# Performance work log

Measured on AMD Instinct MI355X. Metric: run time of the kernel, lower is better.

The kernel has to match this reference:

```python
import jax, jax.numpy as jnp
import numpy as np

N_NODES = 50000
N_EDGES = 800000
N_GRAPHS = 512
D_IN = 128
D_HID = 128
D_OUT = 128
N_CLS = 2


def _deg_inv_sqrt(idx, n):
    deg = jax.ops.segment_sum(jnp.ones(idx.shape[0], jnp.float32), idx, num_segments=n)
    return jnp.where(deg > 0, jax.lax.rsqrt(jnp.maximum(deg, 1.0)), 0.0)


def gcn_conv(x, src, dst, W, b, out_norm, in_norm):
    # DGL GraphConv, norm='both': D_out^{-1/2} on src, sum-aggregate, D_in^{-1/2} on dst, then XW + b
    h = x * out_norm[:, None]                                   # [N, d]
    agg = jax.ops.segment_sum(h[src], dst, num_segments=x.shape[0])  # SpMM: gather + scatter-add
    agg = agg * in_norm[:, None]
    return agg @ W + b


def setup_inputs() -> dict:
    key = jax.random.key(0)
    ks = jax.random.split(key, 8)
    features = jax.random.normal(ks[0], (N_NODES, D_IN), jnp.float32)
    src = jax.random.randint(ks[1], (N_EDGES,), 0, N_NODES, jnp.int32)
    dst = jax.random.randint(ks[2], (N_EDGES,), 0, N_NODES, jnp.int32)
    graph_ids = jnp.sort(jax.random.randint(ks[3], (N_NODES,), 0, N_GRAPHS, jnp.int32))
    W1 = jax.random.normal(ks[4], (D_IN, D_HID), jnp.float32) / np.sqrt(D_IN)
    W2 = jax.random.normal(ks[5], (D_HID, D_OUT), jnp.float32) / np.sqrt(D_HID)
    Wc = jax.random.normal(ks[6], (D_OUT, N_CLS), jnp.float32) / np.sqrt(D_OUT)
    return {
        'features': features, 'src': src, 'dst': dst, 'graph_ids': graph_ids,
        'W1': W1, 'b1': jnp.zeros((D_HID,), jnp.float32),
        'W2': W2, 'b2': jnp.zeros((D_OUT,), jnp.float32),
        'Wc': Wc, 'bc': jnp.zeros((N_CLS,), jnp.float32),
    }


def reference(features, src, dst, graph_ids, W1, b1, W2, b2, Wc, bc):
    n = features.shape[0]
    out_norm = _deg_inv_sqrt(src, n)   # out-degree norm (applied on src side)
    in_norm = _deg_inv_sqrt(dst, n)    # in-degree norm (applied on dst side)
    h = jax.nn.relu(gcn_conv(features, src, dst, W1, b1, out_norm, in_norm))
    h = gcn_conv(h, src, dst, W2, b2, out_norm, in_norm)
    # mean_nodes: segment mean over nodes of each graph
    sums = jax.ops.segment_sum(h, graph_ids, num_segments=N_GRAPHS)          # [G, d]
    cnts = jax.ops.segment_sum(jnp.ones((n,), jnp.float32), graph_ids, num_segments=N_GRAPHS)
    hg = sums / jnp.maximum(cnts, 1.0)[:, None]
    return hg @ Wc + bc
```

## Files before the change

kernel.cpp:

```cpp
#include <hip/hip_runtime.h>
#include <hip/hip_fp16.h>

#define NN 50000
#define NE 800000
#define NG 512
#define DD 128
#define NSB 64
#define SUBN 782
#define SBCAP 14336
#define NB1 512
#define NI4 (NE / 4)
#define CH4 ((NI4 + NB1 - 1) / NB1)
#define F2HB 6250

typedef __attribute__((ext_vector_type(8))) _Float16 f16x8;
typedef __attribute__((ext_vector_type(4))) float f32x4;
typedef int v4i __attribute__((ext_vector_type(4)));

__global__ void k_zero(int* __restrict__ p) {
  p[threadIdx.x] = 0;
}

__global__ __launch_bounds__(256) void k_prep(
    const float* __restrict__ W1, const float* __restrict__ W2,
    const float* __restrict__ Wc, const float* __restrict__ b2,
    const float* __restrict__ bc,
    _Float16* __restrict__ w1hi, _Float16* __restrict__ w1lo,
    float* __restrict__ w2c, float* __restrict__ zc,
    const int* __restrict__ src, const int* __restrict__ dst,
    int* __restrict__ cur_d, int* __restrict__ cur_s,
    unsigned long long* __restrict__ byDst, unsigned short* __restrict__ bySrc,
    const float4* __restrict__ x, uint2* __restrict__ xh) {
  __shared__ int cntd[4][NSB], cnts[4][NSB], based[NSB], bases[NSB];
  __shared__ int wbd[4][NSB], wbs[4][NSB];
  int b = blockIdx.x;
  int tid = threadIdx.x;
  if (b >= 521) {
    int i = (b - 521) * 256 + tid;
    float4 v = x[i];
    __half2 a = __floats2half2_rn(v.x, v.y);
    __half2 c = __floats2half2_rn(v.z, v.w);
    uint2 o;
    o.x = *(unsigned int*)&a;
    o.y = *(unsigned int*)&c;
    xh[i] = o;
  } else if (b < 8) {
    int t = b * 256 + tid;
    int lane = t & 63;
    int grp = t >> 6;
    int kk = grp & 3;
    int nt = grp >> 2;
    int kbase = kk * 32 + ((lane >> 4) << 3);
    int c = nt * 16 + (lane & 15);
#pragma unroll
    for (int j = 0; j < 8; ++j) {
      float v = W1[(kbase + j) * DD + c];
      _Float16 h = (_Float16)v;
      w1hi[t * 8 + j] = h;
      w1lo[t * 8 + j] = (_Float16)(v - (float)h);
    }
  } else if (b == 8) {
    int row = tid >> 1, cc = tid & 1;
    float s = 0.f;
#pragma unroll 8
    for (int c = 0; c < DD; ++c) s += W2[row * DD + c] * Wc[c * 2 + cc];
    w2c[row * 2 + cc] = s;
    if (tid < 2) {
      float bb = 0.f;
      for (int c = 0; c < DD; ++c) bb += b2[c] * Wc[c * 2 + tid];
      zc[tid] = bb + bc[tid];
    }
  } else {
    int w = tid >> 6;
    int i0 = (b - 9) * CH4;
    int i1 = i0 + CH4; if (i1 > NI4) i1 = NI4;
    if (tid < NSB) {
#pragma unroll
      for (int ww = 0; ww < 4; ++ww) { cntd[ww][tid] = 0; cnts[ww][tid] = 0; }
    }
    __syncthreads();
    const v4i* s4 = (const v4i*)src;
    const v4i* d4 = (const v4i*)dst;
    for (int i = i0 + tid; i < i1; i += 256) {
      v4i sv = __builtin_nontemporal_load(&s4[i]);
      v4i dv = __builtin_nontemporal_load(&d4[i]);
#pragma unroll
      for (int k = 0; k < 4; ++k) {
        atomicAdd(&cntd[w][dv[k] / SUBN], 1);
        atomicAdd(&cnts[w][sv[k] / SUBN], 1);
      }
    }
    __syncthreads();
    if (tid < NSB) {
      int run = 0;
#pragma unroll
      for (int ww = 0; ww < 4; ++ww) { wbd[ww][tid] = run; run += cntd[ww][tid]; }
      based[tid] = atomicAdd(&cur_d[tid], run);
#pragma unroll
      for (int ww = 0; ww < 4; ++ww) cntd[ww][tid] = 0;
    } else if (tid < 2 * NSB) {
      int q = tid - NSB;
      int run = 0;
#pragma unroll
      for (int ww = 0; ww < 4; ++ww) { wbs[ww][q] = run; run += cnts[ww][q]; }
      bases[q] = atomicAdd(&cur_s[q], run);
#pragma unroll
      for (int ww = 0; ww < 4; ++ww) cnts[ww][q] = 0;
    }
    __syncthreads();
    for (int i = i0 + tid; i < i1; i += 256) {
      v4i sv = __builtin_nontemporal_load(&s4[i]);
      v4i dv = __builtin_nontemporal_load(&d4[i]);
#pragma unroll
      for (int k = 0; k < 4; ++k) {
        int d = dv[k], s = sv[k];
        int bd = d / SUBN;
        int pd = based[bd] + wbd[w][bd] + atomicAdd(&cntd[w][bd], 1);
        if (pd < SBCAP) byDst[(size_t)bd * SBCAP + pd] = ((unsigned long long)(unsigned)d << 32) | (unsigned)s;
        int bs = s / SUBN;
        int ps = bases[bs] + wbs[w][bs] + atomicAdd(&cnts[w][bs], 1);
        if (ps < SBCAP) bySrc[(size_t)bs * SBCAP + ps] = (unsigned short)(s - bs * SUBN);
      }
    }
  }
}

__global__ __launch_bounds__(1024) void k_csr2(
    const unsigned long long* __restrict__ byDst, const int* __restrict__ cur_d,
    const unsigned short* __restrict__ bySrc, const int* __restrict__ cur_s,
    int* __restrict__ csr, int* __restrict__ row_start, int* __restrict__ deg_in,
    float* __restrict__ in_norm, float* __restrict__ out_norm) {
  __shared__ int hist[SUBN];
  __shared__ int wsum[16];
  int b = blockIdx.x;
  int tid = threadIdx.x;
  if (b < 64) {
    int q = b;
    int nlo = q * SUBN;
    int nhi = nlo + SUBN; if (nhi > NN) nhi = NN;
    int nloc = nhi - nlo;
    for (int i = tid; i < SUBN; i += 1024) hist[i] = 0;
    __syncthreads();
    int m = cur_d[q];
    if (m > SBCAP) m = SBCAP;
    const unsigned long long* bine = byDst + (size_t)q * SBCAP;
    for (int i = tid; i < m; i += 1024) {
      int l = (int)(bine[i] >> 32) - nlo;
      if (l >= 0 && l < nloc) atomicAdd(&hist[l], 1);
    }
    __syncthreads();
    int v = (tid < SUBN) ? hist[tid] : 0;
    int incl = v;
    int lane = tid & 63;
#pragma unroll
    for (int off = 1; off < 64; off <<= 1) {
      int t2 = __shfl_up(incl, off);
      if (lane >= off) incl += t2;
    }
    int wid = tid >> 6;
    if (lane == 63) wsum[wid] = incl;
    __syncthreads();
    if (tid == 0) {
      int run = 0;
      for (int i = 0; i < 16; ++i) { int t = wsum[i]; wsum[i] = run; run += t; }
    }
    __syncthreads();
    int excl = incl - v + wsum[wid];
    if (tid < nloc) {
      deg_in[nlo + tid] = v;
      row_start[nlo + tid] = q * SBCAP + excl;
      in_norm[nlo + tid] = v > 0 ? rsqrtf((float)v) : 0.f;
    }
    __syncthreads();
    if (tid < SUBN) hist[tid] = excl;
    __syncthreads();
    for (int i = tid; i < m; i += 1024) {
      unsigned long long p = bine[i];
      int l = (int)(p >> 32) - nlo;
      if (l >= 0 && l < nloc) {
        int pos = atomicAdd(&hist[l], 1);
        if (pos < SBCAP) csr[(size_t)q * SBCAP + pos] = (int)(unsigned)p;
      }
    }
  } else {
    int q = b - 64;
    int nlo = q * SUBN;
    int nhi = nlo + SUBN; if (nhi > NN) nhi = NN;
    int nloc = nhi - nlo;
    for (int i = tid; i < SUBN; i += 1024) hist[i] = 0;
    __syncthreads();
    int m = cur_s[q];
    if (m > SBCAP) m = SBCAP;
    const unsigned short* bine = bySrc + (size_t)q * SBCAP;
    for (int i = tid; i < m; i += 1024) {
      atomicAdd(&hist[bine[i]], 1);
    }
    __syncthreads();
    for (int i = tid; i < nloc; i += 1024) {
      int od = hist[i];
      out_norm[nlo + i] = od > 0 ? rsqrtf((float)od) : 0.f;
    }
  }
}

__global__ __launch_bounds__(256) void k_agg(
    const __half* __restrict__ x, const int* __restrict__ csr,
    const int* __restrict__ row_start, const int* __restrict__ deg_in,
    const float* __restrict__ out_norm, uint2* __restrict__ agg) {
  int node = blockIdx.x * 4 + (threadIdx.x >> 6);
  int lane = threadIdx.x & 63;
  if (node >= NN) return;
  int n = deg_in[node];
  const int* bk = csr + row_start[node];
  const uint2* xv = (const uint2*)x;
  int half_ = lane >> 5;
  int l32 = lane & 31;
  float4 acc[8];
#pragma unroll
  for (int u = 0; u < 8; ++u) acc[u] = make_float4(0.f, 0.f, 0.f, 0.f);
  for (int c0 = 0; c0 < n; c0 += 64) {
    int nn = n - c0; if (nn > 64) nn = 64;
    int sl = 0; float wl = 0.f;
    if (lane < nn) { sl = bk[c0 + lane]; wl = out_norm[sl]; }
    for (int j = 0; j < nn; j += 16) {
#pragma unroll
      for (int u = 0; u < 8; ++u) {
        int e = j + 2 * u + half_;
        int s = __shfl(sl, e);
        float w = __shfl(wl, e);
        if (e < nn) {
          uint2 raw = xv[(size_t)s * 32 + l32];
          float2 f0 = __half22float2(*(__half2*)&raw.x);
          float2 f1 = __half22float2(*(__half2*)&raw.y);
          acc[u].x += f0.x * w; acc[u].y += f0.y * w;
          acc[u].z += f1.x * w; acc[u].w += f1.y * w;
        }
      }
    }
  }
  float4 a = acc[0];
#pragma unroll
  for (int u = 1; u < 8; ++u) {
    a.x += acc[u].x; a.y += acc[u].y; a.z += acc[u].z; a.w += acc[u].w;
  }
  a.x += __shfl_xor(a.x, 32);
  a.y += __shfl_xor(a.y, 32);
  a.z += __shfl_xor(a.z, 32);
  a.w += __shfl_xor(a.w, 32);
  if (lane < 32) {
    __half2 h0 = __floats2half2_rn(a.x, a.y);
    __half2 h1 = __floats2half2_rn(a.z, a.w);
    uint2 o;
    o.x = *(unsigned int*)&h0;
    o.y = *(unsigned int*)&h1;
    agg[(size_t)node * 32 + l32] = o;
  }
}

__global__ __launch_bounds__(256, 4) void k_gemm1(
    const __half* __restrict__ A, const float* __restrict__ in_norm,
    const float* __restrict__ out_norm,
    const _Float16* __restrict__ Whi, const _Float16* __restrict__ Wlo,
    const float* __restrict__ bias, const float* __restrict__ W2c,
    float2* __restrict__ p) {
  int tid = threadIdx.x;
  int wid = tid >> 6, lane = tid & 63;
  int row0 = blockIdx.x * 64 + wid * 16;
  int ar = row0 + (lane & 15);
  bool rv = ar < NN;
  f16x8 a_[4];
#pragma unroll
  for (int kk = 0; kk < 4; ++kk) {
    if (rv) {
      a_[kk] = *(const f16x8*)((const _Float16*)A + (size_t)ar * DD + kk * 32 + ((lane >> 4) << 3));
    } else {
      a_[kk] = (f16x8){0, 0, 0, 0, 0, 0, 0, 0};
    }
  }
  f32x4 acc[8];
#pragma unroll
  for (int nt = 0; nt < 8; ++nt) acc[nt] = (f32x4){0.f, 0.f, 0.f, 0.f};
#pragma unroll
  for (int nt = 0; nt < 8; ++nt) {
#pragma unroll
    for (int kk = 0; kk < 4; ++kk) {
      f16x8 bh = *(const f16x8*)&Whi[(((nt * 4 + kk) * 64) + lane) * 8];
      f16x8 bl = *(const f16x8*)&Wlo[(((nt * 4 + kk) * 64) + lane) * 8];
      acc[nt] = __builtin_amdgcn_mfma_f32_16x16x32_f16(a_[kk], bh, acc[nt], 0, 0, 0);
      acc[nt] = __builtin_amdgcn_mfma_f32_16x16x32_f16(a_[kk], bl, acc[nt], 0, 0, 0);
    }
  }
  int r4 = (lane >> 4) * 4;
  int c0 = lane & 15;
  float wc0[8], wc1[8], bv[8];
#pragma unroll
  for (int nt = 0; nt < 8; ++nt) {
    int col = nt * 16 + c0;
    wc0[nt] = W2c[col * 2 + 0];
    wc1[nt] = W2c[col * 2 + 1];
    bv[nt] = bias[col];
  }
#pragma unroll
  for (int reg = 0; reg < 4; ++reg) {
    int row = row0 + r4 + reg;
    float inm = (row < NN) ? in_norm[row] : 0.f;
    float v0 = 0.f, v1 = 0.f;
#pragma unroll
    for (int nt = 0; nt < 8; ++nt) {
      float y = acc[nt][reg] * inm + bv[nt];
      y = fmaxf(y, 0.f);
      v0 += y * wc0[nt];
      v1 += y * wc1[nt];
    }
#pragma unroll
    for (int off = 1; off < 16; off <<= 1) {
      v0 += __shfl_xor(v0, off);
      v1 += __shfl_xor(v1, off);
    }
    if (row < NN && c0 == 0) {
      float onm = out_norm[row];
      p[row] = make_float2(v0 * onm, v1 * onm);
    }
  }
}

__global__ __launch_bounds__(256) void k_agg2(
    const float2* __restrict__ p, const int* __restrict__ csr,
    const int* __restrict__ row_start, const int* __restrict__ deg_in,
    const float* __restrict__ in_norm, float2* __restrict__ z) {
  int i = blockIdx.x * 256 + threadIdx.x;
  if (i >= NN) return;
  int n = deg_in[i];
  const int* bk = csr + row_start[i];
  float2 s0 = {0.f, 0.f}, s1 = {0.f, 0.f}, s2 = {0.f, 0.f}, s3 = {0.f, 0.f};
  int j = 0;
  for (; j + 4 <= n; j += 4) {
    int i0 = bk[j], i1 = bk[j + 1], i2 = bk[j + 2], i3 = bk[j + 3];
    float2 q0 = p[i0], q1 = p[i1], q2 = p[i2], q3 = p[i3];
    s0.x += q0.x; s0.y += q0.y;
    s1.x += q1.x; s1.y += q1.y;
    s2.x += q2.x; s2.y += q2.y;
    s3.x += q3.x; s3.y += q3.y;
  }
  for (; j < n; ++j) {
    float2 q = p[bk[j]];
    s0.x += q.x; s0.y += q.y;
  }
  s0.x += s1.x + s2.x + s3.x;
  s0.y += s1.y + s2.y + s3.y;
  float inm = in_norm[i];
  z[i] = make_float2(s0.x * inm, s0.y * inm);
}

__global__ __launch_bounds__(256) void k_pool2(
    const float* __restrict__ z, const int* __restrict__ gid,
    const float* __restrict__ zc, float* __restrict__ out) {
  int g = blockIdx.x * 4 + (threadIdx.x >> 6);
  int lane = threadIdx.x & 63;
  if (g >= NG) return;
  int lo, hi;
  { int a = 0, b = NN; while (a < b) { int m = (a + b) >> 1; if (gid[m] < g) a = m + 1; else b = m; } lo = a; }
  { int a = lo, b = NN; while (a < b) { int m = (a + b) >> 1; if (gid[m] <= g) a = m + 1; else b = m; } hi = a; }
  float s = 0.f;
  int col = lane & 1;
  for (int i = lo + (lane >> 1); i < hi; i += 32) s += z[i * 2 + col];
#pragma unroll
  for (int off = 32; off >= 2; off >>= 1) s += __shfl_down(s, off);
  if (lane < 2) {
    int n = hi - lo;
    out[g * 2 + lane] = s / (float)(n > 0 ? n : 1) + zc[lane];
  }
}

extern "C" void kernel_launch(void* const* d_in, const int* in_sizes, int n_in,
                              void* d_out, int out_size, void* d_ws, size_t ws_size,
                              hipStream_t stream) {
  const float* features = (const float*)d_in[0];
  const int* src = (const int*)d_in[1];
  const int* dst = (const int*)d_in[2];
  const int* gid = (const int*)d_in[3];
  const float* W1 = (const float*)d_in[4];
  const float* b1 = (const float*)d_in[5];
  const float* W2 = (const float*)d_in[6];
  const float* b2 = (const float*)d_in[7];
  const float* Wc = (const float*)d_in[8];
  const float* bc = (const float*)d_in[9];
  float* out = (float*)d_out;

  char* ws = (char*)d_ws;
  size_t off = 0;
  auto take = [&](size_t bytes) {
    char* p = ws + off;
    off = (off + bytes + 255) & ~(size_t)255;
    return p;
  };
  int* cur_d      = (int*)take(NSB * 4);
  int* cur_s      = (int*)take(NSB * 4);
  int* deg_in     = (int*)take((size_t)NN * 4);
  float* out_nrm  = (float*)take((size_t)NN * 4);
  float* in_nrm   = (float*)take((size_t)NN * 4);
  int* row_start  = (int*)take((size_t)NN * 4);
  float* pbuf     = (float*)take((size_t)NN * 2 * 4);
  float* zbuf     = (float*)take((size_t)NN * 2 * 4);
  float* w2c      = (float*)take((size_t)DD * 2 * 4);
  float* zc       = (float*)take(2 * 4);
  unsigned long long* byDst = (unsigned long long*)take((size_t)NSB * SBCAP * 8);
  unsigned short* bySrc = (unsigned short*)take((size_t)NSB * SBCAP * 2);
  int* csr        = (int*)take((size_t)NSB * SBCAP * 4);
  __half* xh      = (__half*)take((size_t)NN * DD * 2);
  __half* bufA    = (__half*)take((size_t)NN * DD * 2);
  _Float16* w1hi  = (_Float16*)take((size_t)DD * DD * 2);
  _Float16* w1lo  = (_Float16*)take((size_t)DD * DD * 2);

  k_zero<<<1, 128, 0, stream>>>(cur_d);

  k_prep<<<521 + F2HB, 256, 0, stream>>>(
      W1, W2, Wc, b2, bc, w1hi, w1lo, w2c, zc,
      src, dst, cur_d, cur_s, byDst, bySrc,
      (const float4*)features, (uint2*)xh);

  k_csr2<<<128, 1024, 0, stream>>>(
      byDst, cur_d, bySrc, cur_s, csr, row_start, deg_in, in_nrm, out_nrm);

  k_agg<<<(NN + 3) / 4, 256, 0, stream>>>(
      xh, csr, row_start, deg_in, out_nrm, (uint2*)bufA);
  k_gemm1<<<(NN + 63) / 64, 256, 0, stream>>>(
      bufA, in_nrm, out_nrm, w1hi, w1lo, b1, w2c, (float2*)pbuf);

  k_agg2<<<(NN + 255) / 256, 256, 0, stream>>>(
      (const float2*)pbuf, csr, row_start, deg_in, in_nrm, (float2*)zbuf);

  k_pool2<<<(NG + 3) / 4, 256, 0, stream>>>(zbuf, gid, zc, out);
}
```

Measured before the change: 122.3 us.

## Map one node per half-wavefront in first-layer aggregation with unrolled gathers

The first-layer SpMM kernel now gives each 32-lane half-wavefront its own destination node, where before a full 64-lane wavefront split one node's edges across two halves and combined them with a cross-half shuffle. Each half walks its node's neighbor list in chunks of 32 and issues eight independent row gathers per step into four accumulators, which should expose more memory-level parallelism. The grid shrinks to half as many blocks of 8 nodes each. Average degree is about 16, so this removes idle lanes and the final reduction, at the cost of possible divergence when the two nodes sharing a wavefront have different degrees.

```diff
diff --git a/kernel.cpp b/kernel.cpp
--- a/kernel.cpp
+++ b/kernel.cpp
@@ -207,49 +207,73 @@
     const __half* __restrict__ x, const int* __restrict__ csr,
     const int* __restrict__ row_start, const int* __restrict__ deg_in,
     const float* __restrict__ out_norm, uint2* __restrict__ agg) {
-  int node = blockIdx.x * 4 + (threadIdx.x >> 6);
-  int lane = threadIdx.x & 63;
-  if (node >= NN) return;
-  int n = deg_in[node];
-  const int* bk = csr + row_start[node];
+  int tid = threadIdx.x;
+  int wid = tid >> 6;
+  int lane = tid & 63;
+  int l32 = lane & 31;
+  int node = blockIdx.x * 8 + wid * 2 + (lane >> 5);
+  bool valid = node < NN;
+  int n = valid ? deg_in[node] : 0;
+  const int* bk = csr + (valid ? row_start[node] : 0);
   const uint2* xv = (const uint2*)x;
-  int half_ = lane >> 5;
-  int l32 = lane & 31;
-  float4 acc[8];
-#pragma unroll
-  for (int u = 0; u < 8; ++u) acc[u] = make_float4(0.f, 0.f, 0.f, 0.f);
-  for (int c0 = 0; c0 < n; c0 += 64) {
-    int nn = n - c0; if (nn > 64) nn = 64;
+  float4 a0 = {0.f,0.f,0.f,0.f}, a1 = {0.f,0.f,0.f,0.f};
+  float4 a2 = {0.f,0.f,0.f,0.f}, a3 = {0.f,0.f,0.f,0.f};
+  for (int c0 = 0; c0 < n; c0 += 32) {
+    int nn = n - c0; if (nn > 32) nn = 32;
     int sl = 0; float wl = 0.f;
-    if (lane < nn) { sl = bk[c0 + lane]; wl = out_norm[sl]; }
-    for (int j = 0; j < nn; j += 16) {
-#pragma unroll
-      for (int u = 0; u < 8; ++u) {
-        int e = j + 2 * u + half_;
-        int s = __shfl(sl, e);
-        float w = __shfl(wl, e);
-        if (e < nn) {
-          uint2 raw = xv[(size_t)s * 32 + l32];
-          float2 f0 = __half22float2(*(__half2*)&raw.x);
-          float2 f1 = __half22float2(*(__half2*)&raw.y);
-          acc[u].x += f0.x * w; acc[u].y += f0.y * w;
-          acc[u].z += f1.x * w; acc[u].w += f1.y * w;
-        }
-      }
-    }
-  }
-  float4 a = acc[0];
-#pragma unroll
-  for (int u = 1; u < 8; ++u) {
-    a.x += acc[u].x; a.y += acc[u].y; a.z += acc[u].z; a.w += acc[u].w;
-  }
-  a.x += __shfl_xor(a.x, 32);
-  a.y += __shfl_xor(a.y, 32);
-  a.z += __shfl_xor(a.z, 32);
-  a.w += __shfl_xor(a.w, 32);
-  if (lane < 32) {
-    __half2 h0 = __floats2half2_rn(a.x, a.y);
-    __half2 h1 = __floats2half2_rn(a.z, a.w);
+    if (l32 < nn) { sl = bk[c0 + l32]; wl = out_norm[sl]; }
+    int j = 0;
+    for (; j + 8 <= nn; j += 8) {
+      int s0 = __shfl(sl, j + 0, 32), s1 = __shfl(sl, j + 1, 32);
+      int s2 = __shfl(sl, j + 2, 32), s3 = __shfl(sl, j + 3, 32);
+      int s4 = __shfl(sl, j + 4, 32), s5 = __shfl(sl, j + 5, 32);
+      int s6 = __shfl(sl, j + 6, 32), s7 = __shfl(sl, j + 7, 32);
+      float w0 = __shfl(wl, j + 0, 32), w1 = __shfl(wl, j + 1, 32);
+      float w2 = __shfl(wl, j + 2, 32), w3 = __shfl(wl, j + 3, 32);
+      float w4 = __shfl(wl, j + 4, 32), w5 = __shfl(wl, j + 5, 32);
+      float w6 = __shfl(wl, j + 6, 32), w7 = __shfl(wl, j + 7, 32);
+      uint2 r0 = xv[(size_t)s0 * 32 + l32];
+      uint2 r1 = xv[(size_t)s1 * 32 + l32];
+      uint2 r2 = xv[(size_t)s2 * 32 + l32];
+      uint2 r3 = xv[(size_t)s3 * 32 + l32];
+      uint2 r4 = xv[(size_t)s4 * 32 + l32];
+      uint2 r5 = xv[(size_t)s5 * 32 + l32];
+      uint2 r6 = xv[(size_t)s6 * 32 + l32];
+      uint2 r7 = xv[(size_t)s7 * 32 + l32];
+      float2 f;
+      f = __half22float2(*(__half2*)&r0.x); a0.x += f.x * w0; a0.y += f.y * w0;
+      f = __half22float2(*(__half2*)&r0.y); a0.z += f.x * w0; a0.w += f.y * w0;
+      f = __half22float2(*(__half2*)&r1.x); a1.x += f.x * w1; a1.y += f.y * w1;
+      f = __half22float2(*(__half2*)&r1.y); a1.z += f.x * w1; a1.w += f.y * w1;
+      f = __half22float2(*(__half2*)&r2.x); a2.x += f.x * w2; a2.y += f.y * w2;
+      f = __half22float2(*(__half2*)&r2.y); a2.z += f.x * w2; a2.w += f.y * w2;
+      f = __half22float2(*(__half2*)&r3.x); a3.x += f.x * w3; a3.y += f.y * w3;
+      f = __half22float2(*(__half2*)&r3.y); a3.z += f.x * w3; a3.w += f.y * w3;
+      f = __half22float2(*(__half2*)&r4.x); a0.x += f.x * w4; a0.y += f.y * w4;
+      f = __half22float2(*(__half2*)&r4.y); a0.z += f.x * w4; a0.w += f.y * w4;
+      f = __half22float2(*(__half2*)&r5.x); a1.x += f.x * w5; a1.y += f.y * w5;
+      f = __half22float2(*(__half2*)&r5.y); a1.z += f.x * w5; a1.w += f.y * w5;
+      f = __half22float2(*(__half2*)&r6.x); a2.x += f.x * w6; a2.y += f.y * w6;
+      f = __half22float2(*(__half2*)&r6.y); a2.z += f.x * w6; a2.w += f.y * w6;
+      f = __half22float2(*(__half2*)&r7.x); a3.x += f.x * w7; a3.y += f.y * w7;
+      f = __half22float2(*(__half2*)&r7.y); a3.z += f.x * w7; a3.w += f.y * w7;
+    }
+    for (; j < nn; ++j) {
+      int s = __shfl(sl, j, 32);
+      float w = __shfl(wl, j, 32);
+      uint2 r = xv[(size_t)s * 32 + l32];
+      float2 f;
+      f = __half22float2(*(__half2*)&r.x); a0.x += f.x * w; a0.y += f.y * w;
+      f = __half22float2(*(__half2*)&r.y); a0.z += f.x * w; a0.w += f.y * w;
+    }
+  }
+  a0.x += a1.x + a2.x + a3.x;
+  a0.y += a1.y + a2.y + a3.y;
+  a0.z += a1.z + a2.z + a3.z;
+  a0.w += a1.w + a2.w + a3.w;
+  if (valid) {
+    __half2 h0 = __floats2half2_rn(a0.x, a0.y);
+    __half2 h1 = __floats2half2_rn(a0.z, a0.w);
     uint2 o;
     o.x = *(unsigned int*)&h0;
     o.y = *(unsigned int*)&h1;
@@ -422,7 +446,7 @@
   k_csr2<<<128, 1024, 0, stream>>>(
       byDst, cur_d, bySrc, cur_s, csr, row_start, deg_in, in_nrm, out_nrm);
 
-  k_agg<<<(NN + 3) / 4, 256, 0, stream>>>(
+  k_agg<<<(NN + 7) / 8, 256, 0, stream>>>(
       xh, csr, row_start, deg_in, out_nrm, (uint2*)bufA);
   k_gemm1<<<(NN + 63) / 64, 256, 0, stream>>>(
       bufA, in_nrm, out_nrm, w1hi, w1lo, b1, w2c, (float2*)pbuf);
```

Result: faster. 110.5 us (-9.6%).
